# Optimization experiments

Measured on AMD Instinct MI355X. Metric: run time of the kernel, lower is better.

Reference implementation:

```python
import jax, jax.numpy as jnp
import numpy as np

B, L = 4, 1024
D_MODEL, D_STATE, D_CONV, EXPAND, NUM_HEADS = 512, 64, 4, 2, 8
HEADDIM = 64
D_INNER = EXPAND * D_MODEL          # 1024
NH = D_INNER // HEADDIM             # 16 SSM heads
D_IN_PROJ = 2 * D_INNER + 2 * D_STATE + NH
CONV_DIM = D_INNER + 2 * D_STATE
D_FF = D_MODEL * EXPAND
ADH = D_MODEL // NUM_HEADS          # attn head dim


def setup_inputs() -> dict:
    ks = iter(jax.random.split(jax.random.key(0), 40))
    def rn(shape, s=0.02):
        return jax.random.normal(next(ks), shape, jnp.float32) * s
    return dict(
        x=jax.random.normal(next(ks), (B, L, D_MODEL), jnp.float32),
        g1=jnp.ones(D_MODEL), b1=jnp.zeros(D_MODEL),
        W_in=rn((D_MODEL, D_IN_PROJ)), b_in=jnp.zeros(D_IN_PROJ),
        conv_w=rn((CONV_DIM, D_CONV), 0.1), conv_b=jnp.zeros(CONV_DIM),
        dt_bias=rn((NH,), 0.1), A_log=jnp.zeros(NH), D_skip=jnp.ones(NH),
        gnorm=jnp.ones(D_INNER),
        W_out=rn((D_INNER, D_MODEL)), b_out=jnp.zeros(D_MODEL),
        ga=jnp.ones(D_MODEL), ba=jnp.zeros(D_MODEL),
        Wqkv=rn((D_MODEL, 3 * D_MODEL)), bqkv=jnp.zeros(3 * D_MODEL),
        Wo=rn((D_MODEL, D_MODEL)), bo=jnp.zeros(D_MODEL),
        g2=jnp.ones(D_MODEL), b2=jnp.zeros(D_MODEL),
        W1=rn((D_MODEL, 2 * D_FF)), b1f=jnp.zeros(2 * D_FF),
        W2=rn((D_FF, D_MODEL)), b2f=jnp.zeros(D_MODEL),
    )


def _ln(x, g, b, eps=1e-5):
    mu = x.mean(-1, keepdims=True)
    v = ((x - mu) ** 2).mean(-1, keepdims=True)
    return (x - mu) * jax.lax.rsqrt(v + eps) * g + b


def _ssm(h, W_in, b_in, conv_w, conv_b, dt_bias, A_log, D_skip, gnorm, W_out, b_out):
    # Mamba2: in_proj -> [z | xBC | dt]
    zxbcdt = h @ W_in + b_in
    z = zxbcdt[..., :D_INNER]
    xBC = zxbcdt[..., D_INNER:D_INNER + CONV_DIM]
    dt = jax.nn.softplus(zxbcdt[..., -NH:] + dt_bias)          # [B,L,H]
    # causal depthwise conv (width D_CONV) + SiLU
    xp = jnp.pad(xBC, ((0, 0), (D_CONV - 1, 0), (0, 0)))
    conv = conv_b + sum(xp[:, k:k + L, :] * conv_w[:, k] for k in range(D_CONV))
    xBC = jax.nn.silu(conv)
    bsz = h.shape[0]
    xs = xBC[..., :D_INNER].reshape(bsz, L, NH, HEADDIM)       # [B,L,H,P]
    Bm = xBC[..., D_INNER:D_INNER + D_STATE]                   # [B,L,N]
    Cm = xBC[..., D_INNER + D_STATE:]                          # [B,L,N]
    dA = jnp.exp(dt * (-jnp.exp(A_log)))                       # [B,L,H]
    dtx = dt[..., None] * xs                                   # [B,L,H,P]

    def step(hs, t):
        dA_t, dtx_t, B_t, C_t = t
        hs = hs * dA_t[..., None, None] + dtx_t[..., None] * B_t[:, None, None, :]
        return hs, jnp.einsum('bhpn,bn->bhp', hs, C_t)

    h0 = jnp.zeros((bsz, NH, HEADDIM, D_STATE), h.dtype)
    _, ys = jax.lax.scan(step, h0, (dA.swapaxes(0, 1), dtx.swapaxes(0, 1),
                                     Bm.swapaxes(0, 1), Cm.swapaxes(0, 1)))
    y = ys.swapaxes(0, 1) + D_skip[None, None, :, None] * xs   # [B,L,H,P]
    y = y.reshape(bsz, L, D_INNER) * jax.nn.silu(z)            # gated
    y = y * jax.lax.rsqrt(jnp.mean(y * y, -1, keepdims=True) + 1e-5) * gnorm  # RMSNormGated
    return y @ W_out + b_out


def _attn(h, Wqkv, bqkv, Wo, bo):
    qkv = h @ Wqkv + bqkv
    q, k, v = jnp.split(qkv, 3, axis=-1)
    bsz = h.shape[0]
    rs = lambda t: t.reshape(bsz, L, NUM_HEADS, ADH)
    q, k, v = rs(q), rs(k), rs(v)
    scale = jnp.float32(1.0 / np.sqrt(ADH))
    att = jax.nn.softmax(jnp.einsum('blhd,bmhd->bhlm', q, k) * scale, axis=-1)
    o = jnp.einsum('bhlm,bmhd->blhd', att, v).reshape(bsz, L, D_MODEL)
    return o @ Wo + bo


def _fwd(x, g1, b1, W_in, b_in, conv_w, conv_b, dt_bias, A_log, D_skip, gnorm,
         W_out, b_out, ga, ba, Wqkv, bqkv, Wo, bo, g2, b2, W1, b1f, W2, b2f):
    x = x + _ssm(_ln(x, g1, b1), W_in, b_in, conv_w, conv_b, dt_bias, A_log,
                 D_skip, gnorm, W_out, b_out)
    x = x + _attn(_ln(x, ga, ba), Wqkv, bqkv, Wo, bo)
    h3 = _ln(x, g2, b2)
    x1, x2 = jnp.split(h3 @ W1 + b1f, 2, axis=-1)
    return x + (jax.nn.gelu(x1, approximate=False) * x2) @ W2 + b2f


def reference(x, g1, b1, W_in, b_in, conv_w, conv_b, dt_bias, A_log, D_skip, gnorm,
              W_out, b_out, ga, ba, Wqkv, bqkv, Wo, bo, g2, b2, W1, b1f, W2, b2f):
    return _fwd(x, g1, b1, W_in, b_in, conv_w, conv_b, dt_bias, A_log, D_skip, gnorm,
                W_out, b_out, ga, ba, Wqkv, bqkv, Wo, bo, g2, b2, W1, b1f, W2, b2f)
```

## Files before the change

kernel.cpp:

```cpp
#include <hip/hip_runtime.h>
#include <hip/hip_bf16.h>
#include <math.h>


#define L_      1024
#define DM      512
#define DSTATE  64
#define DCONV   4
#define DINNER  1024
#define NH_     16
#define DINPROJ 2192
#define CONVDIM 1152
#define ROWS    4096
#define LC      64
#define NC      16

typedef float  f32x4  __attribute__((ext_vector_type(4)));
typedef __bf16 bf16x8 __attribute__((ext_vector_type(8)));
typedef short  short8 __attribute__((ext_vector_type(8)));
using bf16 = __hip_bfloat16;

static __device__ __forceinline__ float b2f(ushort u) { return __uint_as_float((unsigned)u << 16); }
static __device__ __forceinline__ ushort f2b(float f) {
  return __builtin_bit_cast(unsigned short, __float2bfloat16(f));
}
static __device__ __forceinline__ void gload16(const void* g, void* l) {
  __builtin_amdgcn_global_load_lds((const __attribute__((address_space(1))) void*)g,
                                   (__attribute__((address_space(3))) void*)l, 16, 0, 0);
}

struct TcAll {
  const float* W[6];
  ushort* WT[6];
  int K[6], N[6], Nalloc[6], nbx[6], perm[6];
  int start[7];
};
__global__ __launch_bounds__(256) void tcall_k(TcAll d) {
  int bid = blockIdx.x;
  int i = 0;
  #pragma unroll
  for (int t = 1; t < 6; ++t) if (bid >= d.start[t]) i = t;
  int local = bid - d.start[i];
  int bx = (local % d.nbx[i]) * 32, by = (local / d.nbx[i]) * 32;
  const float* W = d.W[i];
  ushort* WT = d.WT[i];
  int K = d.K[i], N = d.N[i], Nalloc = d.Nalloc[i], pm = d.perm[i];
  __shared__ ushort tile[32][33];
  int tx = threadIdx.x & 31, ty = threadIdx.x >> 5;
  #pragma unroll
  for (int r = ty; r < 32; r += 8) {
    int gk = by + r, gn = bx + tx;
    tile[r][tx] = (gk < K && gn < N) ? f2b(W[(size_t)gk * N + gn]) : (ushort)0;
  }
  __syncthreads();
  #pragma unroll
  for (int r = ty; r < 32; r += 8) {
    int gn = bx + r, gk = by + tx;
    if (gn < Nalloc && gk < K) {
      int gn2 = gn;
      if (pm) gn2 = (gn < 1024) ? ((gn >> 4) * 32 + (gn & 15))
                                : (((gn - 1024) >> 4) * 32 + 16 + ((gn - 1024) & 15));
      WT[(size_t)gn2 * K + gk] = tile[tx][r];
    }
  }
}

template <bool COPY>
__global__ __launch_bounds__(256) void ln512t(const float* __restrict__ in, const float* __restrict__ g,
                                              const float* __restrict__ be, bf16* __restrict__ out,
                                              float* __restrict__ rcopy) {
  int row = blockIdx.x, tid = threadIdx.x;
  const float* x = in + (size_t)row * DM;
  float v0 = x[tid], v1 = x[tid + 256];
  if (COPY) {
    rcopy[(size_t)row * DM + tid] = v0;
    rcopy[(size_t)row * DM + tid + 256] = v1;
  }
  float s = v0 + v1, sq = v0 * v0 + v1 * v1;
  __shared__ float red[4][2];
  __shared__ float bc[2];
  int lane = tid & 63, w = tid >> 6;
  #pragma unroll
  for (int o = 32; o; o >>= 1) { s += __shfl_down(s, o); sq += __shfl_down(sq, o); }
  if (lane == 0) { red[w][0] = s; red[w][1] = sq; }
  __syncthreads();
  if (tid == 0) {
    bc[0] = red[0][0] + red[1][0] + red[2][0] + red[3][0];
    bc[1] = red[0][1] + red[1][1] + red[2][1] + red[3][1];
  }
  __syncthreads();
  float mu = bc[0] * (1.f / DM);
  float var = bc[1] * (1.f / DM) - mu * mu;
  float rs = rsqrtf(var + 1e-5f);
  out[(size_t)row * DM + tid] = __float2bfloat16((v0 - mu) * rs * g[tid] + be[tid]);
  out[(size_t)row * DM + tid + 256] =
      __float2bfloat16((v1 - mu) * rs * g[tid + 256] + be[tid + 256]);
}

template <int OMODE, int BM>
__global__ __launch_bounds__(256) void gemmT(const ushort* __restrict__ A, long lda, long sA1,
                                             const ushort* __restrict__ Bw, long ldb, long sB1,
                                             const float* __restrict__ bias,
                                             void* __restrict__ Cp, long ldc, long sC1,
                                             const float* __restrict__ Rp,
                                             int M, int N, int K, float scale) {
  constexpr int MFR = BM / 32;
  __shared__ ushort As[BM * 64];
  __shared__ ushort Bs[128 * 64];
  const int tid = threadIdx.x;
  const int z = blockIdx.z;
  A  += (size_t)z * sA1;
  Bw += (size_t)z * sB1;
  const int m0 = blockIdx.y * BM, n0 = blockIdx.x * 128;
  const int wave = tid >> 6, lane = tid & 63;
  const int wr = wave >> 1, wc = wave & 1;
  const int frow = lane & 15, fgrp = lane >> 4;

  f32x4 acc[MFR][4];
  #pragma unroll
  for (int m = 0; m < MFR; ++m)
    #pragma unroll
    for (int n = 0; n < 4; ++n) acc[m][n] = {0.f, 0.f, 0.f, 0.f};

  for (int kt = 0; kt < K; kt += 64) {
    #pragma unroll
    for (int it = 0; it < MFR; ++it) {
      int idx = it * 256 + tid;
      int row = idx >> 3, seg = idx & 7;
      gload16(A + (size_t)(m0 + row) * lda + kt + seg * 8, &As[idx * 8]);
    }
    #pragma unroll
    for (int it = 0; it < 4; ++it) {
      int idx = it * 256 + tid;
      int row = idx >> 3, seg = idx & 7;
      gload16(Bw + (size_t)(n0 + row) * ldb + kt + seg * 8, &Bs[idx * 8]);
    }
    __syncthreads();
    #pragma unroll
    for (int kk = 0; kk < 64; kk += 32) {
      bf16x8 af[MFR], bfr[4];
      #pragma unroll
      for (int m = 0; m < MFR; ++m)
        af[m] = *(const bf16x8*)&As[(wr * (BM / 2) + m * 16 + frow) * 64 + kk + 8 * fgrp];
      #pragma unroll
      for (int n = 0; n < 4; ++n)
        bfr[n] = *(const bf16x8*)&Bs[(wc * 64 + n * 16 + frow) * 64 + kk + 8 * fgrp];
      #pragma unroll
      for (int m = 0; m < MFR; ++m)
        #pragma unroll
        for (int n = 0; n < 4; ++n)
          acc[m][n] = __builtin_amdgcn_mfma_f32_16x16x32_bf16(af[m], bfr[n], acc[m][n], 0, 0, 0);
    }
    __syncthreads();
  }

  if (OMODE == 1) {
    #pragma unroll
    for (int jp = 0; jp < 2; ++jp) {
      int oc = n0 / 2 + wc * 32 + jp * 16 + frow;
      float b1v = bias[oc], b2v = bias[1024 + oc];
      #pragma unroll
      for (int m = 0; m < MFR; ++m) {
        #pragma unroll
        for (int r = 0; r < 4; ++r) {
          int gm = m0 + wr * (BM / 2) + m * 16 + fgrp * 4 + r;
          float x1 = acc[m][jp * 2][r] + b1v;
          float x2 = acc[m][jp * 2 + 1][r] + b2v;
          float g = 0.5f * x1 * (1.f + erff(x1 * 0.70710678f));
          ((bf16*)Cp)[(size_t)gm * ldc + oc] = __float2bfloat16(g * x2);
        }
      }
    }
    return;
  }
  #pragma unroll
  for (int n = 0; n < 4; ++n) {
    int gn = n0 + wc * 64 + n * 16 + frow;
    if (gn >= N) continue;
    float bv = bias ? bias[gn] : 0.f;
    #pragma unroll
    for (int m = 0; m < MFR; ++m) {
      #pragma unroll
      for (int r = 0; r < 4; ++r) {
        int gm = m0 + wr * (BM / 2) + m * 16 + fgrp * 4 + r;
        float v = acc[m][n][r] * scale + bv;
        size_t off = (size_t)z * sC1 + (size_t)gm * ldc + gn;
        if (OMODE == 0)      ((bf16*)Cp)[off] = __float2bfloat16(v);
        else if (OMODE == 2) ((float*)Cp)[off] += v;
        else                 ((float*)Cp)[off] = Rp[off] + v;
      }
    }
  }
}

__global__ __launch_bounds__(256) void fattn_k(const ushort* __restrict__ qkv,
                                               const ushort* __restrict__ VT,
                                               float* __restrict__ Opart,
                                               float* __restrict__ lpart) {
  const int qt = blockIdx.x, bh = blockIdx.y, z = blockIdx.z, b = bh >> 3, hh = bh & 7;
  const int tid = threadIdx.x, wave = tid >> 6, lane = tid & 63;
  const int frow = lane & 15, fgrp = lane >> 4;
  __shared__ __align__(16) ushort QP_lds[64][72];
  __shared__ __align__(16) ushort K_lds[2][64][72];
  __shared__ __align__(16) ushort V_lds[2][64][72];
  const int q0 = qt * 64;
  const int kv0 = z * 8;
  const int r0 = tid >> 3, r1 = r0 + 32, sg = (tid & 7) * 8;

  *(short8*)&QP_lds[r0][sg] = *(const short8*)(qkv + (size_t)(b * L_ + q0 + r0) * 1536 + hh * 64 + sg);
  *(short8*)&QP_lds[r1][sg] = *(const short8*)(qkv + (size_t)(b * L_ + q0 + r1) * 1536 + hh * 64 + sg);
  __syncthreads();
  bf16x8 qf[2];
  qf[0] = *(const bf16x8*)&QP_lds[wave * 16 + frow][0 + 8 * fgrp];
  qf[1] = *(const bf16x8*)&QP_lds[wave * 16 + frow][32 + 8 * fgrp];

  float l_r[4] = {0.f, 0.f, 0.f, 0.f};
  f32x4 o_acc[4];
  #pragma unroll
  for (int j = 0; j < 4; ++j) o_acc[j] = {0.f, 0.f, 0.f, 0.f};

  short8 kr0, kr1, vr0, vr1;
  {
    const ushort* kp = qkv + (size_t)(b * L_ + kv0 * 64) * 1536 + 512 + hh * 64;
    kr0 = *(const short8*)(kp + (size_t)r0 * 1536 + sg);
    kr1 = *(const short8*)(kp + (size_t)r1 * 1536 + sg);
    const ushort* vp = VT + (size_t)bh * 65536 + kv0 * 64;
    vr0 = *(const short8*)(vp + (size_t)r0 * 1024 + sg);
    vr1 = *(const short8*)(vp + (size_t)r1 * 1024 + sg);
  }

  for (int kv = kv0; kv < kv0 + 8; ++kv) {
    const int cur = kv & 1;
    *(short8*)&K_lds[cur][r0][sg] = kr0;
    *(short8*)&K_lds[cur][r1][sg] = kr1;
    *(short8*)&V_lds[cur][r0][sg] = vr0;
    *(short8*)&V_lds[cur][r1][sg] = vr1;
    __syncthreads();
    if (kv < kv0 + 7) {
      const ushort* kp = qkv + (size_t)(b * L_ + (kv + 1) * 64) * 1536 + 512 + hh * 64;
      kr0 = *(const short8*)(kp + (size_t)r0 * 1536 + sg);
      kr1 = *(const short8*)(kp + (size_t)r1 * 1536 + sg);
      const ushort* vp = VT + (size_t)bh * 65536 + (kv + 1) * 64;
      vr0 = *(const short8*)(vp + (size_t)r0 * 1024 + sg);
      vr1 = *(const short8*)(vp + (size_t)r1 * 1024 + sg);
    }

    f32x4 s[4];
    #pragma unroll
    for (int j = 0; j < 4; ++j) s[j] = {0.f, 0.f, 0.f, 0.f};
    #pragma unroll
    for (int kk = 0; kk < 2; ++kk) {
      bf16x8 a = qf[kk];
      #pragma unroll
      for (int j = 0; j < 4; ++j) {
        bf16x8 bb = *(const bf16x8*)&K_lds[cur][j * 16 + frow][kk * 32 + 8 * fgrp];
        s[j] = __builtin_amdgcn_mfma_f32_16x16x32_bf16(a, bb, s[j], 0, 0, 0);
      }
    }
    #pragma unroll
    for (int r = 0; r < 4; ++r) {
      #pragma unroll
      for (int j = 0; j < 4; ++j) {
        float p = expf(s[j][r] * 0.125f);
        s[j][r] = p;
        l_r[r] += p;
      }
    }
    #pragma unroll
    for (int r = 0; r < 4; ++r)
      #pragma unroll
      for (int j = 0; j < 4; ++j)
        QP_lds[wave * 16 + fgrp * 4 + r][j * 16 + frow] = f2b(s[j][r]);
    #pragma unroll
    for (int kk = 0; kk < 2; ++kk) {
      bf16x8 pa = *(const bf16x8*)&QP_lds[wave * 16 + frow][kk * 32 + 8 * fgrp];
      #pragma unroll
      for (int j = 0; j < 4; ++j) {
        bf16x8 bb = *(const bf16x8*)&V_lds[cur][j * 16 + frow][kk * 32 + 8 * fgrp];
        o_acc[j] = __builtin_amdgcn_mfma_f32_16x16x32_bf16(pa, bb, o_acc[j], 0, 0, 0);
      }
    }
  }
  #pragma unroll
  for (int r = 0; r < 4; ++r) {
    #pragma unroll
    for (int o = 1; o < 16; o <<= 1) l_r[r] += __shfl_xor(l_r[r], o);
  }
  float* Op = Opart + (size_t)z * ROWS * DM;
  #pragma unroll
  for (int r = 0; r < 4; ++r) {
    int orow = q0 + wave * 16 + fgrp * 4 + r;
    #pragma unroll
    for (int j = 0; j < 4; ++j)
      Op[(size_t)(b * L_ + orow) * DM + hh * 64 + j * 16 + frow] = o_acc[j][r];
    if (frow == 0) lpart[(size_t)z * ROWS * 8 + (size_t)(b * L_ + orow) * 8 + hh] = l_r[r];
  }
}

__global__ __launch_bounds__(256) void fcomb_k(const float* __restrict__ Opart,
                                               const float* __restrict__ lpart,
                                               bf16* __restrict__ Out) {
  int i = blockIdx.x * 256 + threadIdx.x;
  int row = i >> 7, c4 = (i & 127) * 4;
  f32x4 o0 = *(const f32x4*)&Opart[(size_t)row * DM + c4];
  f32x4 o1 = *(const f32x4*)&Opart[(size_t)ROWS * DM + (size_t)row * DM + c4];
  int hh = c4 >> 6;
  float l = lpart[(size_t)row * 8 + hh] + lpart[(size_t)ROWS * 8 + (size_t)row * 8 + hh];
  float inv = 1.f / l;
  ushort4 o;
  o.x = f2b((o0[0] + o1[0]) * inv);
  o.y = f2b((o0[1] + o1[1]) * inv);
  o.z = f2b((o0[2] + o1[2]) * inv);
  o.w = f2b((o0[3] + o1[3]) * inv);
  *(ushort4*)&Out[(size_t)row * DM + c4] = o;
}

__global__ __launch_bounds__(256) void convk(const ushort* __restrict__ zx, const float* __restrict__ cw,
                                             const float* __restrict__ cb, ushort* __restrict__ xbc) {
  int i = blockIdx.x * 256 + threadIdx.x;
  if (i >= ROWS * CONVDIM) return;
  int c = i % CONVDIM;
  int t = (i / CONVDIM) & (L_ - 1);
  int b = i / (CONVDIM * L_);
  float acc = cb[c];
  #pragma unroll
  for (int k = 0; k < DCONV; ++k) {
    int ts = t + k - (DCONV - 1);
    if (ts >= 0)
      acc += b2f(zx[(size_t)(b * L_ + ts) * DINPROJ + DINNER + c]) * cw[c * DCONV + k];
  }
  xbc[i] = f2b(acc / (1.f + expf(-acc)));
}

__global__ __launch_bounds__(256) void scanA_k(const ushort* __restrict__ xbc,
                                               const ushort* __restrict__ zx,
                                               const float* __restrict__ dtb,
                                               const float* __restrict__ alog,
                                               ushort* __restrict__ Sbuf,
                                               float* __restrict__ Pbuf,
                                               float* __restrict__ laBuf,
                                               float* __restrict__ dtBuf) {
  const int c = blockIdx.x, bh = blockIdx.y, b = bh >> 4, hh = bh & 15;
  const int tid = threadIdx.x, wave = tid >> 6, lane = tid & 63;
  const int frow = lane & 15, fgrp = lane >> 4;
  const int t0 = c * LC;
  __shared__ __align__(16) ushort XT[64][72];
  __shared__ __align__(16) ushort BT[64][72];
  __shared__ float sw[64];

  if (tid < 64) {
    int row = b * L_ + t0 + tid;
    float v = b2f(zx[(size_t)row * DINPROJ + (DINPROJ - NH_) + hh]) + dtb[hh];
    float d = (v > 20.f) ? v : log1pf(expf(v));
    float la = -expf(alog[hh]) * d;
    #pragma unroll
    for (int off = 1; off < 64; off <<= 1) {
      float u = __shfl_up(la, off);
      if (tid >= off) la += u;
    }
    float la63 = __shfl(la, 63);
    sw[tid] = d * expf(la63 - la);
    laBuf[((size_t)bh * NC + c) * 64 + tid] = la;
    dtBuf[((size_t)bh * NC + c) * 64 + tid] = d;
    if (tid == 63) Pbuf[bh * NC + c] = expf(la);
  }
  __syncthreads();

  {
    int t = tid >> 2, ch0 = (tid & 3) * 16;
    size_t base = (size_t)(b * L_ + t0 + t) * CONVDIM;
    short8 x0 = *(const short8*)&xbc[base + hh * 64 + ch0];
    short8 x1 = *(const short8*)&xbc[base + hh * 64 + ch0 + 8];
    short8 b0 = *(const short8*)&xbc[base + DINNER + ch0];
    short8 b1 = *(const short8*)&xbc[base + DINNER + ch0 + 8];
    float wt = sw[t];
    #pragma unroll
    for (int j = 0; j < 8; ++j) {
      XT[ch0 + j][t]     = f2b(b2f((ushort)x0[j]) * wt);
      XT[ch0 + 8 + j][t] = f2b(b2f((ushort)x1[j]) * wt);
      BT[ch0 + j][t]     = (ushort)b0[j];
      BT[ch0 + 8 + j][t] = (ushort)b1[j];
    }
  }
  __syncthreads();

  f32x4 acc[4];
  #pragma unroll
  for (int j = 0; j < 4; ++j) acc[j] = {0.f, 0.f, 0.f, 0.f};
  #pragma unroll
  for (int kk = 0; kk < 2; ++kk) {
    bf16x8 a = *(const bf16x8*)&XT[wave * 16 + frow][kk * 32 + 8 * fgrp];
    #pragma unroll
    for (int j = 0; j < 4; ++j) {
      bf16x8 bb = *(const bf16x8*)&BT[j * 16 + frow][kk * 32 + 8 * fgrp];
      acc[j] = __builtin_amdgcn_mfma_f32_16x16x32_bf16(a, bb, acc[j], 0, 0, 0);
    }
  }
  ushort* Sp = Sbuf + ((size_t)bh * NC + c) * 4096;
  #pragma unroll
  for (int j = 0; j < 4; ++j)
    #pragma unroll
    for (int r = 0; r < 4; ++r)
      Sp[(wave * 16 + fgrp * 4 + r) * 64 + j * 16 + frow] = f2b(acc[j][r]);
}

__global__ __launch_bounds__(256) void scan2_k(ushort* __restrict__ Sbuf, const float* __restrict__ Pbuf) {
  int bh = blockIdx.x, tid = threadIdx.x;
  float H[16];
  #pragma unroll
  for (int i = 0; i < 16; ++i) H[i] = 0.f;
  for (int c = 0; c < NC - 1; ++c) {
    ushort* Sp = Sbuf + ((size_t)bh * NC + c) * 4096 + tid * 16;
    float P = Pbuf[bh * NC + c];
    short8 a = *(short8*)Sp, b = *(short8*)(Sp + 8);
    #pragma unroll
    for (int j = 0; j < 8; ++j) {
      H[j]     = H[j]     * P + b2f((ushort)a[j]);
      H[8 + j] = H[8 + j] * P + b2f((ushort)b[j]);
    }
    short8 w0, w1;
    #pragma unroll
    for (int j = 0; j < 8; ++j) { w0[j] = (short)f2b(H[j]); w1[j] = (short)f2b(H[8 + j]); }
    *(short8*)Sp = w0;
    *(short8*)(Sp + 8) = w1;
  }
}

__global__ __launch_bounds__(256) void scanB_k(const ushort* __restrict__ xbc,
                                               const float* __restrict__ Dskip,
                                               const ushort* __restrict__ Sbuf,
                                               const float* __restrict__ laBuf,
                                               const float* __restrict__ dtBuf,
                                               ushort* __restrict__ yb) {
  const int c = blockIdx.x, bh = blockIdx.y, b = bh >> 4, hh = bh & 15;
  const int tid = threadIdx.x, wave = tid >> 6, lane = tid & 63;
  const int frow = lane & 15, fgrp = lane >> 4;
  const int t0 = c * LC;
  __shared__ __align__(16) ushort C_l[64][72];
  __shared__ __align__(16) ushort BH[64][72];
  __shared__ __align__(16) ushort XT[64][72];
  __shared__ __align__(16) ushort M_l[64][72];
  __shared__ float sla[64], sdt[64];

  if (tid < 64) {
    sla[tid] = laBuf[((size_t)bh * NC + c) * 64 + tid];
    sdt[tid] = dtBuf[((size_t)bh * NC + c) * 64 + tid];
  }
  {
    int t = tid >> 2, ch0 = (tid & 3) * 16;
    size_t base = (size_t)(b * L_ + t0 + t) * CONVDIM;
    short8 c0 = *(const short8*)&xbc[base + DINNER + DSTATE + ch0];
    short8 c1 = *(const short8*)&xbc[base + DINNER + DSTATE + ch0 + 8];
    *(short8*)&C_l[t][ch0] = c0;
    *(short8*)&C_l[t][ch0 + 8] = c1;
    short8 b0 = *(const short8*)&xbc[base + DINNER + ch0];
    short8 b1 = *(const short8*)&xbc[base + DINNER + ch0 + 8];
    *(short8*)&BH[t][ch0] = b0;
    *(short8*)&BH[t][ch0 + 8] = b1;
    short8 x0 = *(const short8*)&xbc[base + hh * 64 + ch0];
    short8 x1 = *(const short8*)&xbc[base + hh * 64 + ch0 + 8];
    #pragma unroll
    for (int j = 0; j < 8; ++j) {
      XT[ch0 + j][t]     = (ushort)x0[j];
      XT[ch0 + 8 + j][t] = (ushort)x1[j];
    }
  }
  __syncthreads();

  f32x4 g[4];
  #pragma unroll
  for (int j = 0; j < 4; ++j) g[j] = {0.f, 0.f, 0.f, 0.f};
  #pragma unroll
  for (int kk = 0; kk < 2; ++kk) {
    bf16x8 a = *(const bf16x8*)&C_l[wave * 16 + frow][kk * 32 + 8 * fgrp];
    #pragma unroll
    for (int j = 0; j < 4; ++j) {
      bf16x8 bb = *(const bf16x8*)&BH[j * 16 + frow][kk * 32 + 8 * fgrp];
      g[j] = __builtin_amdgcn_mfma_f32_16x16x32_bf16(a, bb, g[j], 0, 0, 0);
    }
  }
  #pragma unroll
  for (int r = 0; r < 4; ++r) {
    int trow = wave * 16 + fgrp * 4 + r;
    float lat = sla[trow];
    #pragma unroll
    for (int j = 0; j < 4; ++j) {
      int scol = j * 16 + frow;
      float m = (scol <= trow) ? expf(lat - sla[scol]) * sdt[scol] * g[j][r] : 0.f;
      M_l[trow][scol] = f2b(m);
    }
  }
  __syncthreads();
  {
    int p = tid >> 2, n0 = (tid & 3) * 16;
    if (c > 0) {
      const ushort* Hp = Sbuf + ((size_t)bh * NC + (c - 1)) * 4096 + p * 64 + n0;
      *(short8*)&BH[p][n0] = *(const short8*)Hp;
      *(short8*)&BH[p][n0 + 8] = *(const short8*)(Hp + 8);
    } else {
      short8 zz;
      #pragma unroll
      for (int j = 0; j < 8; ++j) zz[j] = 0;
      *(short8*)&BH[p][n0] = zz;
      *(short8*)&BH[p][n0 + 8] = zz;
    }
  }
  __syncthreads();

  f32x4 y1[4], y2[4];
  #pragma unroll
  for (int j = 0; j < 4; ++j) { y1[j] = {0.f, 0.f, 0.f, 0.f}; y2[j] = {0.f, 0.f, 0.f, 0.f}; }
  #pragma unroll
  for (int kk = 0; kk < 2; ++kk) {
    bf16x8 am = *(const bf16x8*)&M_l[wave * 16 + frow][kk * 32 + 8 * fgrp];
    bf16x8 ac = *(const bf16x8*)&C_l[wave * 16 + frow][kk * 32 + 8 * fgrp];
    #pragma unroll
    for (int j = 0; j < 4; ++j) {
      bf16x8 bx = *(const bf16x8*)&XT[j * 16 + frow][kk * 32 + 8 * fgrp];
      bf16x8 bhf = *(const bf16x8*)&BH[j * 16 + frow][kk * 32 + 8 * fgrp];
      y1[j] = __builtin_amdgcn_mfma_f32_16x16x32_bf16(am, bx, y1[j], 0, 0, 0);
      y2[j] = __builtin_amdgcn_mfma_f32_16x16x32_bf16(ac, bhf, y2[j], 0, 0, 0);
    }
  }
  float dsk = Dskip[hh];
  #pragma unroll
  for (int r = 0; r < 4; ++r) {
    int trow = wave * 16 + fgrp * 4 + r;
    float ea = expf(sla[trow]);
    size_t orow = (size_t)(b * L_ + t0 + trow) * DINNER + hh * 64;
    #pragma unroll
    for (int j = 0; j < 4; ++j) {
      int pcol = j * 16 + frow;
      float y = y1[j][r] + ea * y2[j][r] + dsk * b2f(XT[pcol][trow]);
      yb[orow + pcol] = f2b(y);
    }
  }
}

__global__ __launch_bounds__(256) void grms_k(const ushort* __restrict__ yb, const ushort* __restrict__ zx,
                                              const float* __restrict__ gn, bf16* __restrict__ out) {
  int row = blockIdx.x, tid = threadIdx.x;
  const ushort* y = yb + (size_t)row * DINNER;
  const ushort* z = zx + (size_t)row * DINPROJ;
  float v[4], sq = 0.f;
  #pragma unroll
  for (int k = 0; k < 4; ++k) {
    int c = tid + k * 256;
    float zz = b2f(z[c]);
    float val = b2f(y[c]) * (zz / (1.f + expf(-zz)));
    v[k] = val;
    sq += val * val;
  }
  __shared__ float red[4];
  __shared__ float bc;
  int lane = tid & 63, w = tid >> 6;
  #pragma unroll
  for (int o = 32; o; o >>= 1) sq += __shfl_down(sq, o);
  if (lane == 0) red[w] = sq;
  __syncthreads();
  if (tid == 0) bc = red[0] + red[1] + red[2] + red[3];
  __syncthreads();
  float rs = rsqrtf(bc * (1.f / DINNER) + 1e-5f);
  #pragma unroll
  for (int k = 0; k < 4; ++k) {
    int c = tid + k * 256;
    out[(size_t)row * DINNER + c] = __float2bfloat16(v[k] * rs * gn[c]);
  }
}

__global__ __launch_bounds__(256) void vt_k(const ushort* __restrict__ qkv, ushort* __restrict__ VT) {
  int bh = blockIdx.z, b = bh >> 3, hh = bh & 7;
  int m0 = blockIdx.x * 32, d0 = blockIdx.y * 32;
  __shared__ ushort tile[32][33];
  int tx = threadIdx.x & 31, ty = threadIdx.x >> 5;
  #pragma unroll
  for (int r = ty; r < 32; r += 8)
    tile[r][tx] = qkv[(size_t)(b * L_ + m0 + r) * 1536 + 1024 + hh * 64 + d0 + tx];
  __syncthreads();
  #pragma unroll
  for (int r = ty; r < 32; r += 8)
    VT[(size_t)bh * 65536 + (size_t)(d0 + r) * 1024 + m0 + tx] = tile[tx][r];
}

extern "C" void kernel_launch(void* const* d_in, const int* in_sizes, int n_in,
                              void* d_out, int out_size, void* d_ws, size_t ws_size,
                              hipStream_t stream) {
  const float* x_in = (const float*)d_in[0];
  const float* g1   = (const float*)d_in[1];
  const float* b1   = (const float*)d_in[2];
  const float* b_in = (const float*)d_in[4];
  const float* cw   = (const float*)d_in[5];
  const float* cb   = (const float*)d_in[6];
  const float* dtb  = (const float*)d_in[7];
  const float* alog = (const float*)d_in[8];
  const float* dsk  = (const float*)d_in[9];
  const float* gno  = (const float*)d_in[10];
  const float* bout = (const float*)d_in[12];
  const float* ga   = (const float*)d_in[13];
  const float* ba   = (const float*)d_in[14];
  const float* bqkv = (const float*)d_in[16];
  const float* bo   = (const float*)d_in[18];
  const float* g2   = (const float*)d_in[19];
  const float* b2   = (const float*)d_in[20];
  const float* b1f  = (const float*)d_in[22];
  const float* b2f_ = (const float*)d_in[24];

  char* ws = (char*)d_ws;
  ushort* WT_in  = (ushort*)(ws + 0);
  ushort* WT_out = (ushort*)(ws + 2359296);
  ushort* WT_qkv = (ushort*)(ws + 3407872);
  ushort* WT_o   = (ushort*)(ws + 4980736);
  ushort* WT_1   = (ushort*)(ws + 5505024);
  ushort* WT_2   = (ushort*)(ws + 7602176);
  float*  r   = (float*)(ws + 8650752);
  bf16*   h   = (bf16*)(ws + 17039360);
  ushort* zx  = (ushort*)(ws + 21233664);
  ushort* xbc = (ushort*)(ws + 39190528);
  ushort* yb  = (ushort*)(ws + 49152000);
  bf16*   hy  = (bf16*)(ws + 57540608);
  ushort* qkv = zx;
  ushort* Sbuf = (ushort*)hy;
  ushort* VT   = (ushort*)hy;
  float*  Pbuf  = (float*)h;
  float*  laBuf = (float*)((char*)h + 65536);
  float*  dtBuf = (float*)((char*)h + 327680);
  float*  Opart = (float*)(ws + 39190528);
  float*  lpart = (float*)(ws + 55967744);

  TcAll tc;
  tc.W[0] = (const float*)d_in[3];  tc.WT[0] = WT_in;  tc.K[0] = 512;  tc.N[0] = 2192; tc.Nalloc[0] = 2304; tc.nbx[0] = 72; tc.perm[0] = 0;
  tc.W[1] = (const float*)d_in[11]; tc.WT[1] = WT_out; tc.K[1] = 1024; tc.N[1] = 512;  tc.Nalloc[1] = 512;  tc.nbx[1] = 16; tc.perm[1] = 0;
  tc.W[2] = (const float*)d_in[15]; tc.WT[2] = WT_qkv; tc.K[2] = 512;  tc.N[2] = 1536; tc.Nalloc[2] = 1536; tc.nbx[2] = 48; tc.perm[2] = 0;
  tc.W[3] = (const float*)d_in[17]; tc.WT[3] = WT_o;   tc.K[3] = 512;  tc.N[3] = 512;  tc.Nalloc[3] = 512;  tc.nbx[3] = 16; tc.perm[3] = 0;
  tc.W[4] = (const float*)d_in[21]; tc.WT[4] = WT_1;   tc.K[4] = 512;  tc.N[4] = 2048; tc.Nalloc[4] = 2048; tc.nbx[4] = 64; tc.perm[4] = 1;
  tc.W[5] = (const float*)d_in[23]; tc.WT[5] = WT_2;   tc.K[5] = 1024; tc.N[5] = 512;  tc.Nalloc[5] = 512;  tc.nbx[5] = 16; tc.perm[5] = 0;
  tc.start[0] = 0;    tc.start[1] = 1152; tc.start[2] = 1664; tc.start[3] = 2432;
  tc.start[4] = 2688; tc.start[5] = 3712; tc.start[6] = 4224;
  tcall_k<<<4224, 256, 0, stream>>>(tc);

  ln512t<true><<<ROWS, 256, 0, stream>>>(x_in, g1, b1, h, r);
  gemmT<0, 128><<<dim3(18, 32, 1), 256, 0, stream>>>((const ushort*)h, 512, 0, WT_in, 512, 0,
                                                     b_in, zx, 2192, 0, nullptr, 4096, 2192, 512, 1.f);
  convk<<<18432, 256, 0, stream>>>(zx, cw, cb, xbc);
  scanA_k<<<dim3(NC, 64), 256, 0, stream>>>(xbc, zx, dtb, alog, Sbuf, Pbuf, laBuf, dtBuf);
  scan2_k<<<64, 256, 0, stream>>>(Sbuf, Pbuf);
  scanB_k<<<dim3(NC, 64), 256, 0, stream>>>(xbc, dsk, Sbuf, laBuf, dtBuf, yb);
  grms_k<<<ROWS, 256, 0, stream>>>(yb, zx, gno, hy);
  gemmT<2, 64><<<dim3(4, 64, 1), 256, 0, stream>>>((const ushort*)hy, 1024, 0, WT_out, 1024, 0,
                                                   bout, r, 512, 0, nullptr, 4096, 512, 1024, 1.f);
  ln512t<false><<<ROWS, 256, 0, stream>>>(r, ga, ba, h, nullptr);
  gemmT<0, 128><<<dim3(12, 32, 1), 256, 0, stream>>>((const ushort*)h, 512, 0, WT_qkv, 512, 0,
                                                     bqkv, qkv, 1536, 0, nullptr, 4096, 1536, 512, 1.f);
  vt_k<<<dim3(32, 2, 32), 256, 0, stream>>>(qkv, (ushort*)VT);
  fattn_k<<<dim3(16, 32, 2), 256, 0, stream>>>(qkv, (const ushort*)VT, Opart, lpart);
  fcomb_k<<<2048, 256, 0, stream>>>(Opart, lpart, h);
  gemmT<2, 64><<<dim3(4, 64, 1), 256, 0, stream>>>((const ushort*)h, 512, 0, WT_o, 512, 0,
                                                   bo, r, 512, 0, nullptr, 4096, 512, 512, 1.f);
  ln512t<false><<<ROWS, 256, 0, stream>>>(r, g2, b2, h, nullptr);
  gemmT<1, 128><<<dim3(16, 32, 1), 256, 0, stream>>>((const ushort*)h, 512, 0, WT_1, 512, 0,
                                                     b1f, hy, 1024, 0, nullptr, 4096, 2048, 512, 1.f);
  gemmT<3, 64><<<dim3(4, 64, 1), 256, 0, stream>>>((const ushort*)hy, 1024, 0, WT_2, 1024, 0,
                                                   b2f_, d_out, 512, 0, r, 4096, 512, 1024, 1.f);
}
```

Measured before the change: 253.2 us.

## Fuse causal conv into scan kernels and process two query tiles per attention block

Removes the standalone depthwise conv+SiLU kernel and its xbc buffer, recomputing the conv from zx inside scanA_k and scanB_k using per-block cached weights. Separately, fattn_k now handles 128 query rows per block (two 64-row sub-tiles), reusing each loaded K/V tile twice and halving the grid. This cuts global traffic and a launch, at the cost of redundant conv arithmetic and extra loads in the scans, and fewer attention blocks with higher register pressure.

```diff
diff --git a/kernel.cpp b/kernel.cpp
--- a/kernel.cpp
+++ b/kernel.cpp
@@ -203,21 +203,29 @@
   __shared__ __align__(16) ushort QP_lds[64][72];
   __shared__ __align__(16) ushort K_lds[2][64][72];
   __shared__ __align__(16) ushort V_lds[2][64][72];
-  const int q0 = qt * 64;
+  const int q0 = qt * 128;
   const int kv0 = z * 8;
   const int r0 = tid >> 3, r1 = r0 + 32, sg = (tid & 7) * 8;
 
-  *(short8*)&QP_lds[r0][sg] = *(const short8*)(qkv + (size_t)(b * L_ + q0 + r0) * 1536 + hh * 64 + sg);
-  *(short8*)&QP_lds[r1][sg] = *(const short8*)(qkv + (size_t)(b * L_ + q0 + r1) * 1536 + hh * 64 + sg);
-  __syncthreads();
-  bf16x8 qf[2];
-  qf[0] = *(const bf16x8*)&QP_lds[wave * 16 + frow][0 + 8 * fgrp];
-  qf[1] = *(const bf16x8*)&QP_lds[wave * 16 + frow][32 + 8 * fgrp];
-
-  float l_r[4] = {0.f, 0.f, 0.f, 0.f};
-  f32x4 o_acc[4];
-  #pragma unroll
-  for (int j = 0; j < 4; ++j) o_acc[j] = {0.f, 0.f, 0.f, 0.f};
+  *(short8*)&K_lds[0][r0][sg] = *(const short8*)(qkv + (size_t)(b * L_ + q0 + r0) * 1536 + hh * 64 + sg);
+  *(short8*)&K_lds[0][r1][sg] = *(const short8*)(qkv + (size_t)(b * L_ + q0 + r1) * 1536 + hh * 64 + sg);
+  *(short8*)&K_lds[1][r0][sg] = *(const short8*)(qkv + (size_t)(b * L_ + q0 + 64 + r0) * 1536 + hh * 64 + sg);
+  *(short8*)&K_lds[1][r1][sg] = *(const short8*)(qkv + (size_t)(b * L_ + q0 + 64 + r1) * 1536 + hh * 64 + sg);
+  __syncthreads();
+  bf16x8 qf[2][2];
+  #pragma unroll
+  for (int q2 = 0; q2 < 2; ++q2) {
+    qf[q2][0] = *(const bf16x8*)&K_lds[q2][wave * 16 + frow][0 + 8 * fgrp];
+    qf[q2][1] = *(const bf16x8*)&K_lds[q2][wave * 16 + frow][32 + 8 * fgrp];
+  }
+  __syncthreads();
+
+  float l_r[2][4] = {{0.f, 0.f, 0.f, 0.f}, {0.f, 0.f, 0.f, 0.f}};
+  f32x4 o_acc[2][4];
+  #pragma unroll
+  for (int q2 = 0; q2 < 2; ++q2)
+    #pragma unroll
+    for (int j = 0; j < 4; ++j) o_acc[q2][j] = {0.f, 0.f, 0.f, 0.f};
 
   short8 kr0, kr1, vr0, vr1;
   {
@@ -245,55 +253,58 @@
       vr1 = *(const short8*)(vp + (size_t)r1 * 1024 + sg);
     }
 
-    f32x4 s[4];
-    #pragma unroll
-    for (int j = 0; j < 4; ++j) s[j] = {0.f, 0.f, 0.f, 0.f};
-    #pragma unroll
-    for (int kk = 0; kk < 2; ++kk) {
-      bf16x8 a = qf[kk];
-      #pragma unroll
-      for (int j = 0; j < 4; ++j) {
-        bf16x8 bb = *(const bf16x8*)&K_lds[cur][j * 16 + frow][kk * 32 + 8 * fgrp];
-        s[j] = __builtin_amdgcn_mfma_f32_16x16x32_bf16(a, bb, s[j], 0, 0, 0);
+    #pragma unroll
+    for (int q2 = 0; q2 < 2; ++q2) {
+      f32x4 s[4];
+      #pragma unroll
+      for (int j = 0; j < 4; ++j) s[j] = {0.f, 0.f, 0.f, 0.f};
+      #pragma unroll
+      for (int kk = 0; kk < 2; ++kk) {
+        bf16x8 a = qf[q2][kk];
+        #pragma unroll
+        for (int j = 0; j < 4; ++j) {
+          bf16x8 bb = *(const bf16x8*)&K_lds[cur][j * 16 + frow][kk * 32 + 8 * fgrp];
+          s[j] = __builtin_amdgcn_mfma_f32_16x16x32_bf16(a, bb, s[j], 0, 0, 0);
+        }
       }
-    }
+      #pragma unroll
+      for (int r = 0; r < 4; ++r) {
+        #pragma unroll
+        for (int j = 0; j < 4; ++j) {
+          float p = expf(s[j][r] * 0.125f);
+          s[j][r] = p;
+          l_r[q2][r] += p;
+        }
+      }
+      #pragma unroll
+      for (int r = 0; r < 4; ++r)
+        #pragma unroll
+        for (int j = 0; j < 4; ++j)
+          QP_lds[wave * 16 + fgrp * 4 + r][j * 16 + frow] = f2b(s[j][r]);
+      #pragma unroll
+      for (int kk = 0; kk < 2; ++kk) {
+        bf16x8 pa = *(const bf16x8*)&QP_lds[wave * 16 + frow][kk * 32 + 8 * fgrp];
+        #pragma unroll
+        for (int j = 0; j < 4; ++j) {
+          bf16x8 bb = *(const bf16x8*)&V_lds[cur][j * 16 + frow][kk * 32 + 8 * fgrp];
+          o_acc[q2][j] = __builtin_amdgcn_mfma_f32_16x16x32_bf16(pa, bb, o_acc[q2][j], 0, 0, 0);
+        }
+      }
+    }
+  }
+  float* Op = Opart + (size_t)z * ROWS * DM;
+  #pragma unroll
+  for (int q2 = 0; q2 < 2; ++q2) {
     #pragma unroll
     for (int r = 0; r < 4; ++r) {
       #pragma unroll
-      for (int j = 0; j < 4; ++j) {
-        float p = expf(s[j][r] * 0.125f);
-        s[j][r] = p;
-        l_r[r] += p;
-      }
-    }
-    #pragma unroll
-    for (int r = 0; r < 4; ++r)
+      for (int o = 1; o < 16; o <<= 1) l_r[q2][r] += __shfl_xor(l_r[q2][r], o);
+      int orow = q0 + q2 * 64 + wave * 16 + fgrp * 4 + r;
       #pragma unroll
       for (int j = 0; j < 4; ++j)
-        QP_lds[wave * 16 + fgrp * 4 + r][j * 16 + frow] = f2b(s[j][r]);
-    #pragma unroll
-    for (int kk = 0; kk < 2; ++kk) {
-      bf16x8 pa = *(const bf16x8*)&QP_lds[wave * 16 + frow][kk * 32 + 8 * fgrp];
-      #pragma unroll
-      for (int j = 0; j < 4; ++j) {
-        bf16x8 bb = *(const bf16x8*)&V_lds[cur][j * 16 + frow][kk * 32 + 8 * fgrp];
-        o_acc[j] = __builtin_amdgcn_mfma_f32_16x16x32_bf16(pa, bb, o_acc[j], 0, 0, 0);
-      }
-    }
-  }
-  #pragma unroll
-  for (int r = 0; r < 4; ++r) {
-    #pragma unroll
-    for (int o = 1; o < 16; o <<= 1) l_r[r] += __shfl_xor(l_r[r], o);
-  }
-  float* Op = Opart + (size_t)z * ROWS * DM;
-  #pragma unroll
-  for (int r = 0; r < 4; ++r) {
-    int orow = q0 + wave * 16 + fgrp * 4 + r;
-    #pragma unroll
-    for (int j = 0; j < 4; ++j)
-      Op[(size_t)(b * L_ + orow) * DM + hh * 64 + j * 16 + frow] = o_acc[j][r];
-    if (frow == 0) lpart[(size_t)z * ROWS * 8 + (size_t)(b * L_ + orow) * 8 + hh] = l_r[r];
+        Op[(size_t)(b * L_ + orow) * DM + hh * 64 + j * 16 + frow] = o_acc[q2][j][r];
+      if (frow == 0) lpart[(size_t)z * ROWS * 8 + (size_t)(b * L_ + orow) * 8 + hh] = l_r[q2][r];
+    }
   }
 }
 
@@ -315,25 +326,33 @@
   *(ushort4*)&Out[(size_t)row * DM + c4] = o;
 }
 
-__global__ __launch_bounds__(256) void convk(const ushort* __restrict__ zx, const float* __restrict__ cw,
-                                             const float* __restrict__ cb, ushort* __restrict__ xbc) {
-  int i = blockIdx.x * 256 + threadIdx.x;
-  if (i >= ROWS * CONVDIM) return;
-  int c = i % CONVDIM;
-  int t = (i / CONVDIM) & (L_ - 1);
-  int b = i / (CONVDIM * L_);
-  float acc = cb[c];
-  #pragma unroll
-  for (int k = 0; k < DCONV; ++k) {
-    int ts = t + k - (DCONV - 1);
-    if (ts >= 0)
-      acc += b2f(zx[(size_t)(b * L_ + ts) * DINPROJ + DINNER + c]) * cw[c * DCONV + k];
-  }
-  xbc[i] = f2b(acc / (1.f + expf(-acc)));
-}
-
-__global__ __launch_bounds__(256) void scanA_k(const ushort* __restrict__ xbc,
-                                               const ushort* __restrict__ zx,
+
+static __device__ __forceinline__ void conv16(const ushort* __restrict__ zx, int b, int tglob,
+                                              int zcol, const float (*cw4)[4], const float* cbs,
+                                              float* out) {
+  #pragma unroll
+  for (int j = 0; j < 16; ++j) out[j] = cbs[j];
+  #pragma unroll
+  for (int k = 0; k < 4; ++k) {
+    int ts = tglob + k - 3;
+    if (ts >= 0) {
+      const ushort* rp = zx + (size_t)(b * L_ + ts) * DINPROJ + zcol;
+      short8 v0 = *(const short8*)rp;
+      short8 v1 = *(const short8*)(rp + 8);
+      #pragma unroll
+      for (int j = 0; j < 8; ++j) {
+        out[j]     += b2f((ushort)v0[j]) * cw4[j][k];
+        out[8 + j] += b2f((ushort)v1[j]) * cw4[8 + j][k];
+      }
+    }
+  }
+  #pragma unroll
+  for (int j = 0; j < 16; ++j) out[j] = out[j] / (1.f + expf(-out[j]));
+}
+
+__global__ __launch_bounds__(256) void scanA_k(const ushort* __restrict__ zx,
+                                               const float* __restrict__ cw,
+                                               const float* __restrict__ cb,
                                                const float* __restrict__ dtb,
                                                const float* __restrict__ alog,
                                                ushort* __restrict__ Sbuf,
@@ -347,10 +366,18 @@
   __shared__ __align__(16) ushort XT[64][72];
   __shared__ __align__(16) ushort BT[64][72];
   __shared__ float sw[64];
-
+  __shared__ float cw4[128][4];
+  __shared__ float cbs[128];
+
+  if (tid < 128) {
+    int conv_c = (tid < 64) ? (hh * 64 + tid) : (960 + tid);
+    float4 w = *(const float4*)&cw[conv_c * 4];
+    cw4[tid][0] = w.x; cw4[tid][1] = w.y; cw4[tid][2] = w.z; cw4[tid][3] = w.w;
+    cbs[tid] = cb[conv_c];
+  }
   if (tid < 64) {
     int row = b * L_ + t0 + tid;
-    float v = b2f(zx[(size_t)row * DINPROJ + (DINPROJ - NH_) + hh]) + dtb[hh];
+    float v = b2f(zx[(size_t)row * DINPROJ + (DINPROJ - NH_) + tid * 0 + hh]) + dtb[hh];
     float d = (v > 20.f) ? v : log1pf(expf(v));
     float la = -expf(alog[hh]) * d;
     #pragma unroll
@@ -368,18 +395,14 @@
 
   {
     int t = tid >> 2, ch0 = (tid & 3) * 16;
-    size_t base = (size_t)(b * L_ + t0 + t) * CONVDIM;
-    short8 x0 = *(const short8*)&xbc[base + hh * 64 + ch0];
-    short8 x1 = *(const short8*)&xbc[base + hh * 64 + ch0 + 8];
-    short8 b0 = *(const short8*)&xbc[base + DINNER + ch0];
-    short8 b1 = *(const short8*)&xbc[base + DINNER + ch0 + 8];
+    float xv[16], bv[16];
+    conv16(zx, b, t0 + t, DINNER + hh * 64 + ch0, &cw4[ch0], &cbs[ch0], xv);
+    conv16(zx, b, t0 + t, DINNER + 1024 + ch0, &cw4[64 + ch0], &cbs[64 + ch0], bv);
     float wt = sw[t];
     #pragma unroll
-    for (int j = 0; j < 8; ++j) {
-      XT[ch0 + j][t]     = f2b(b2f((ushort)x0[j]) * wt);
-      XT[ch0 + 8 + j][t] = f2b(b2f((ushort)x1[j]) * wt);
-      BT[ch0 + j][t]     = (ushort)b0[j];
-      BT[ch0 + 8 + j][t] = (ushort)b1[j];
+    for (int j = 0; j < 16; ++j) {
+      XT[ch0 + j][t] = f2b(xv[j] * wt);
+      BT[ch0 + j][t] = f2b(bv[j]);
     }
   }
   __syncthreads();
@@ -426,7 +449,9 @@
   }
 }
 
-__global__ __launch_bounds__(256) void scanB_k(const ushort* __restrict__ xbc,
+__global__ __launch_bounds__(256) void scanB_k(const ushort* __restrict__ zx,
+                                               const float* __restrict__ cw,
+                                               const float* __restrict__ cb,
                                                const float* __restrict__ Dskip,
                                                const ushort* __restrict__ Sbuf,
                                                const float* __restrict__ laBuf,
@@ -441,28 +466,31 @@
   __shared__ __align__(16) ushort XT[64][72];
   __shared__ __align__(16) ushort M_l[64][72];
   __shared__ float sla[64], sdt[64];
-
+  __shared__ float cw4[192][4];
+  __shared__ float cbs[192];
+
+  if (tid < 192) {
+    int conv_c = (tid < 64) ? (hh * 64 + tid) : (960 + tid);
+    float4 w = *(const float4*)&cw[conv_c * 4];
+    cw4[tid][0] = w.x; cw4[tid][1] = w.y; cw4[tid][2] = w.z; cw4[tid][3] = w.w;
+    cbs[tid] = cb[conv_c];
+  }
   if (tid < 64) {
     sla[tid] = laBuf[((size_t)bh * NC + c) * 64 + tid];
     sdt[tid] = dtBuf[((size_t)bh * NC + c) * 64 + tid];
   }
+  __syncthreads();
   {
     int t = tid >> 2, ch0 = (tid & 3) * 16;
-    size_t base = (size_t)(b * L_ + t0 + t) * CONVDIM;
-    short8 c0 = *(const short8*)&xbc[base + DINNER + DSTATE + ch0];
-    short8 c1 = *(const short8*)&xbc[base + DINNER + DSTATE + ch0 + 8];
-    *(short8*)&C_l[t][ch0] = c0;
-    *(short8*)&C_l[t][ch0 + 8] = c1;
-    short8 b0 = *(const short8*)&xbc[base + DINNER + ch0];
-    short8 b1 = *(const short8*)&xbc[base + DINNER + ch0 + 8];
-    *(short8*)&BH[t][ch0] = b0;
-    *(short8*)&BH[t][ch0 + 8] = b1;
-    short8 x0 = *(const short8*)&xbc[base + hh * 64 + ch0];
-    short8 x1 = *(const short8*)&xbc[base + hh * 64 + ch0 + 8];
-    #pragma unroll
-    for (int j = 0; j < 8; ++j) {
-      XT[ch0 + j][t]     = (ushort)x0[j];
-      XT[ch0 + 8 + j][t] = (ushort)x1[j];
+    float xv[16], bv[16], cv[16];
+    conv16(zx, b, t0 + t, DINNER + hh * 64 + ch0, &cw4[ch0], &cbs[ch0], xv);
+    conv16(zx, b, t0 + t, DINNER + 1024 + ch0, &cw4[64 + ch0], &cbs[64 + ch0], bv);
+    conv16(zx, b, t0 + t, DINNER + 1088 + ch0, &cw4[128 + ch0], &cbs[128 + ch0], cv);
+    #pragma unroll
+    for (int j = 0; j < 16; ++j) {
+      C_l[t][ch0 + j] = f2b(cv[j]);
+      BH[t][ch0 + j]  = f2b(bv[j]);
+      XT[ch0 + j][t]  = f2b(xv[j]);
     }
   }
   __syncthreads();
@@ -615,7 +643,6 @@
   float*  r   = (float*)(ws + 8650752);
   bf16*   h   = (bf16*)(ws + 17039360);
   ushort* zx  = (ushort*)(ws + 21233664);
-  ushort* xbc = (ushort*)(ws + 39190528);
   ushort* yb  = (ushort*)(ws + 49152000);
   bf16*   hy  = (bf16*)(ws + 57540608);
   ushort* qkv = zx;
@@ -641,10 +668,9 @@
   ln512t<true><<<ROWS, 256, 0, stream>>>(x_in, g1, b1, h, r);
   gemmT<0, 128><<<dim3(18, 32, 1), 256, 0, stream>>>((const ushort*)h, 512, 0, WT_in, 512, 0,
                                                      b_in, zx, 2192, 0, nullptr, 4096, 2192, 512, 1.f);
-  convk<<<18432, 256, 0, stream>>>(zx, cw, cb, xbc);
-  scanA_k<<<dim3(NC, 64), 256, 0, stream>>>(xbc, zx, dtb, alog, Sbuf, Pbuf, laBuf, dtBuf);
+  scanA_k<<<dim3(NC, 64), 256, 0, stream>>>(zx, cw, cb, dtb, alog, Sbuf, Pbuf, laBuf, dtBuf);
   scan2_k<<<64, 256, 0, stream>>>(Sbuf, Pbuf);
-  scanB_k<<<dim3(NC, 64), 256, 0, stream>>>(xbc, dsk, Sbuf, laBuf, dtBuf, yb);
+  scanB_k<<<dim3(NC, 64), 256, 0, stream>>>(zx, cw, cb, dsk, Sbuf, laBuf, dtBuf, yb);
   grms_k<<<ROWS, 256, 0, stream>>>(yb, zx, gno, hy);
   gemmT<2, 64><<<dim3(4, 64, 1), 256, 0, stream>>>((const ushort*)hy, 1024, 0, WT_out, 1024, 0,
                                                    bout, r, 512, 0, nullptr, 4096, 512, 1024, 1.f);
@@ -652,7 +678,7 @@
   gemmT<0, 128><<<dim3(12, 32, 1), 256, 0, stream>>>((const ushort*)h, 512, 0, WT_qkv, 512, 0,
                                                      bqkv, qkv, 1536, 0, nullptr, 4096, 1536, 512, 1.f);
   vt_k<<<dim3(32, 2, 32), 256, 0, stream>>>(qkv, (ushort*)VT);
-  fattn_k<<<dim3(16, 32, 2), 256, 0, stream>>>(qkv, (const ushort*)VT, Opart, lpart);
+  fattn_k<<<dim3(8, 32, 2), 256, 0, stream>>>(qkv, (const ushort*)VT, Opart, lpart);
   fcomb_k<<<2048, 256, 0, stream>>>(Opart, lpart, h);
   gemmT<2, 64><<<dim3(4, 64, 1), 256, 0, stream>>>((const ushort*)h, 512, 0, WT_o, 512, 0,
                                                    bo, r, 512, 0, nullptr, 4096, 512, 512, 1.f);
```

After: 261.1 us. 3.1% more time.

## Fold inter-chunk state scan into scanB by recomputing prefix per block

Applied to the files above, without the earlier changes.

Removes the separate scan2_k launch that serially propagated chunk states. Each scanB block now recomputes its incoming state by looping over all previous chunks' local states and decay factors, keeping the running state in registers. This saves a kernel launch and the serial 64-block pass with its global read-modify-write, at the cost of redundant reads. Chunk c reads c earlier states, so total traffic grows roughly quadratically in the chunk count (16 chunks). It also avoids rounding intermediate states to bf16.

```diff
diff --git a/kernel.cpp b/kernel.cpp
--- a/kernel.cpp
+++ b/kernel.cpp
@@ -404,31 +404,10 @@
       Sp[(wave * 16 + fgrp * 4 + r) * 64 + j * 16 + frow] = f2b(acc[j][r]);
 }
 
-__global__ __launch_bounds__(256) void scan2_k(ushort* __restrict__ Sbuf, const float* __restrict__ Pbuf) {
-  int bh = blockIdx.x, tid = threadIdx.x;
-  float H[16];
-  #pragma unroll
-  for (int i = 0; i < 16; ++i) H[i] = 0.f;
-  for (int c = 0; c < NC - 1; ++c) {
-    ushort* Sp = Sbuf + ((size_t)bh * NC + c) * 4096 + tid * 16;
-    float P = Pbuf[bh * NC + c];
-    short8 a = *(short8*)Sp, b = *(short8*)(Sp + 8);
-    #pragma unroll
-    for (int j = 0; j < 8; ++j) {
-      H[j]     = H[j]     * P + b2f((ushort)a[j]);
-      H[8 + j] = H[8 + j] * P + b2f((ushort)b[j]);
-    }
-    short8 w0, w1;
-    #pragma unroll
-    for (int j = 0; j < 8; ++j) { w0[j] = (short)f2b(H[j]); w1[j] = (short)f2b(H[8 + j]); }
-    *(short8*)Sp = w0;
-    *(short8*)(Sp + 8) = w1;
-  }
-}
-
 __global__ __launch_bounds__(256) void scanB_k(const ushort* __restrict__ xbc,
                                                const float* __restrict__ Dskip,
                                                const ushort* __restrict__ Sbuf,
+                                               const float* __restrict__ Pbuf,
                                                const float* __restrict__ laBuf,
                                                const float* __restrict__ dtBuf,
                                                ushort* __restrict__ yb) {
@@ -465,6 +444,23 @@
       XT[ch0 + 8 + j][t] = (ushort)x1[j];
     }
   }
+  float Hreg[16];
+  #pragma unroll
+  for (int j = 0; j < 16; ++j) Hreg[j] = 0.f;
+  {
+    int p = tid >> 2, n0 = (tid & 3) * 16;
+    for (int cc = 0; cc < c; ++cc) {
+      const ushort* Sp = Sbuf + ((size_t)bh * NC + cc) * 4096 + p * 64 + n0;
+      float P = Pbuf[bh * NC + cc];
+      short8 a = *(const short8*)Sp;
+      short8 bq = *(const short8*)(Sp + 8);
+      #pragma unroll
+      for (int j = 0; j < 8; ++j) {
+        Hreg[j]     = Hreg[j]     * P + b2f((ushort)a[j]);
+        Hreg[8 + j] = Hreg[8 + j] * P + b2f((ushort)bq[j]);
+      }
+    }
+  }
   __syncthreads();
 
   f32x4 g[4];
@@ -493,17 +489,11 @@
   __syncthreads();
   {
     int p = tid >> 2, n0 = (tid & 3) * 16;
-    if (c > 0) {
-      const ushort* Hp = Sbuf + ((size_t)bh * NC + (c - 1)) * 4096 + p * 64 + n0;
-      *(short8*)&BH[p][n0] = *(const short8*)Hp;
-      *(short8*)&BH[p][n0 + 8] = *(const short8*)(Hp + 8);
-    } else {
-      short8 zz;
-      #pragma unroll
-      for (int j = 0; j < 8; ++j) zz[j] = 0;
-      *(short8*)&BH[p][n0] = zz;
-      *(short8*)&BH[p][n0 + 8] = zz;
-    }
+    short8 w0, w1;
+    #pragma unroll
+    for (int j = 0; j < 8; ++j) { w0[j] = (short)f2b(Hreg[j]); w1[j] = (short)f2b(Hreg[8 + j]); }
+    *(short8*)&BH[p][n0] = w0;
+    *(short8*)&BH[p][n0 + 8] = w1;
   }
   __syncthreads();
 
@@ -643,8 +633,7 @@
                                                      b_in, zx, 2192, 0, nullptr, 4096, 2192, 512, 1.f);
   convk<<<18432, 256, 0, stream>>>(zx, cw, cb, xbc);
   scanA_k<<<dim3(NC, 64), 256, 0, stream>>>(xbc, zx, dtb, alog, Sbuf, Pbuf, laBuf, dtBuf);
-  scan2_k<<<64, 256, 0, stream>>>(Sbuf, Pbuf);
-  scanB_k<<<dim3(NC, 64), 256, 0, stream>>>(xbc, dsk, Sbuf, laBuf, dtBuf, yb);
+  scanB_k<<<dim3(NC, 64), 256, 0, stream>>>(xbc, dsk, Sbuf, Pbuf, laBuf, dtBuf, yb);
   grms_k<<<ROWS, 256, 0, stream>>>(yb, zx, gno, hy);
   gemmT<2, 64><<<dim3(4, 64, 1), 256, 0, stream>>>((const ushort*)hy, 1024, 0, WT_out, 1024, 0,
                                                    bout, r, 512, 0, nullptr, 4096, 512, 1024, 1.f);
```

New measurement: 251.6 us. About the same (-0.7%).
